# Optimization experiments

Measured on AMD Instinct MI355X. Metric: run time of the kernel, lower is better.

## Reference

```python
import jax, jax.numpy as jnp
import numpy as np
from itertools import combinations

B, F, E, V = 4096, 39, 40, 1000000
BN_EPS = 1e-3  # tf.layers.batch_normalization default epsilon


def setup_inputs() -> dict:
    key = jax.random.key(0)
    k_in, k_w, k_v, k_e = jax.random.split(key, 4)
    inputs = jax.random.randint(k_in, (B, F), 0, V, dtype=jnp.int64)
    # generate_pairs(range(F)): cols = first elements, rows = second elements
    pairs = np.array(list(combinations(range(F), 2)), dtype=np.int64)  # [741, 2]
    cols = jnp.asarray(pairs[:, 0])
    rows = jnp.asarray(pairs[:, 1])
    w = jax.random.normal(k_w, (V,), dtype=jnp.float32) * 0.01
    v = jax.random.normal(k_v, (V, E), dtype=jnp.float32) * (1.0 / np.sqrt(E))
    b = jnp.zeros((), dtype=jnp.float32)
    # edge weights init ~ uniform(weight_base - 1e-3, weight_base + 1e-3)
    edge_weights = jax.random.uniform(k_e, (pairs.shape[0],), dtype=jnp.float32,
                                      minval=0.599, maxval=0.601)
    return {"inputs": inputs, "rows": rows, "cols": cols,
            "w": w, "v": v, "b": b, "edge_weights": edge_weights}


def reference(inputs, rows, cols, w, v, b, edge_weights):
    # Embedding lookups
    xw = w[inputs]                      # [B, F]  first-order weights
    xv = v[inputs]                      # [B, F, E] second-order embeddings
    l = jnp.sum(xw, axis=1)             # [B] linear term

    # Pairwise FM interactions: gather field pairs, multiply, reduce over embed
    left = xv[:, rows]                  # [B, P, E]
    right = xv[:, cols]                 # [B, P, E]
    level_2 = jnp.sum(left * right, axis=-1)  # [B, P]

    # BatchNorm (training mode, scale=False, center=False): batch stats per pair
    mean = jnp.mean(level_2, axis=0)
    var = jnp.var(level_2, axis=0)      # biased variance, as in TF BN
    level_2 = (level_2 - mean) * jax.lax.rsqrt(var + BN_EPS)

    # Edge-weight (architecture) mask
    level_2 = level_2 * edge_weights[None, :]

    fm_out = jnp.sum(level_2, axis=-1)  # [B]
    logits = l + fm_out + b             # [B]
    return logits
```

## Files before the change

### kernel.cpp

```cpp
#include <hip/hip_runtime.h>

#define NF 39
#define NE 40
#define NB 4096
#define NSLOT 1536
#define NBLK 512
#define SPW 2
#define SPB 8
#define K2_BLOCKS 48
#define EPS 1.0e-3f

typedef __attribute__((ext_vector_type(8))) short short8;
typedef __attribute__((ext_vector_type(4))) float floatx4;

__device__ __forceinline__ unsigned int f2bf(float f) {
    unsigned int b = __float_as_uint(f);
    b += 0x7FFFu + ((b >> 16) & 1u);
    return b >> 16;
}

__device__ __forceinline__ short8 pack8(float4 a, float4 b) {
    union { unsigned int u[4]; short8 s; } o;
    o.u[0] = f2bf(a.x) | (f2bf(a.y) << 16);
    o.u[1] = f2bf(a.z) | (f2bf(a.w) << 16);
    o.u[2] = f2bf(b.x) | (f2bf(b.y) << 16);
    o.u[3] = f2bf(b.z) | (f2bf(b.w) << 16);
    return o.s;
}

__device__ __forceinline__ void load_frags(
    const int* __restrict__ ip, const float* __restrict__ v,
    int rbase, int ehalf, short8 F0[3], short8 F1[3])
{
    const float4 zero4 = {0.f, 0.f, 0.f, 0.f};
#pragma unroll
    for (int I = 0; I < 3; ++I) {
        const int r = rbase + 16 * I;
        const bool vr = (r < NF);
        const int id = vr ? ip[r] : 0;
        const float* vrow = v + (size_t)id * NE;
        const float4 a  = vr ? *reinterpret_cast<const float4*>(vrow + ehalf * 8)     : zero4;
        const float4 bq = vr ? *reinterpret_cast<const float4*>(vrow + ehalf * 8 + 4) : zero4;
        F0[I] = pack8(a, bq);
        const bool v1 = vr && (ehalf == 0);
        const float4 c_ = v1 ? *reinterpret_cast<const float4*>(vrow + 32) : zero4;
        const float4 d_ = v1 ? *reinterpret_cast<const float4*>(vrow + 36) : zero4;
        F1[I] = pack8(c_, d_);
    }
}

__device__ __forceinline__ void gram_mfma(const short8 F0[3], const short8 F1[3], floatx4 acc[6])
{
    acc[0] = __builtin_amdgcn_mfma_f32_16x16x32_bf16(F0[0], F0[0], acc[0], 0, 0, 0);
    acc[1] = __builtin_amdgcn_mfma_f32_16x16x32_bf16(F0[0], F0[1], acc[1], 0, 0, 0);
    acc[2] = __builtin_amdgcn_mfma_f32_16x16x32_bf16(F0[0], F0[2], acc[2], 0, 0, 0);
    acc[3] = __builtin_amdgcn_mfma_f32_16x16x32_bf16(F0[1], F0[1], acc[3], 0, 0, 0);
    acc[4] = __builtin_amdgcn_mfma_f32_16x16x32_bf16(F0[1], F0[2], acc[4], 0, 0, 0);
    acc[5] = __builtin_amdgcn_mfma_f32_16x16x32_bf16(F0[2], F0[2], acc[5], 0, 0, 0);
    acc[0] = __builtin_amdgcn_mfma_f32_16x16x32_bf16(F1[0], F1[0], acc[0], 0, 0, 0);
    acc[1] = __builtin_amdgcn_mfma_f32_16x16x32_bf16(F1[0], F1[1], acc[1], 0, 0, 0);
    acc[2] = __builtin_amdgcn_mfma_f32_16x16x32_bf16(F1[0], F1[2], acc[2], 0, 0, 0);
    acc[3] = __builtin_amdgcn_mfma_f32_16x16x32_bf16(F1[1], F1[1], acc[3], 0, 0, 0);
    acc[4] = __builtin_amdgcn_mfma_f32_16x16x32_bf16(F1[1], F1[2], acc[4], 0, 0, 0);
    acc[5] = __builtin_amdgcn_mfma_f32_16x16x32_bf16(F1[2], F1[2], acc[5], 0, 0, 0);
}

__global__ __launch_bounds__(256) void fm_k1(
    const int* __restrict__ inputs, const float* __restrict__ w,
    const float* __restrict__ v, short8* __restrict__ wf0,
    short8* __restrict__ wf1, float* __restrict__ lsum,
    float* __restrict__ partial)
{
    __shared__ float red[4 * 2 * NSLOT];
    const int t = threadIdx.x, wid = t >> 6, lane = t & 63;
    const int rbase = lane & 15, ehalf = lane >> 4;
    const int b0 = blockIdx.x * SPB;

    floatx4 sum[6] = {}, sq[6] = {};
#pragma unroll
    for (int s = 0; s < SPW; ++s) {
        const int smp = b0 + wid * SPW + s;
        const int* ip = inputs + (size_t)smp * NF;
        short8 F0[3], F1[3];
        load_frags(ip, v, rbase, ehalf, F0, F1);
#pragma unroll
        for (int I = 0; I < 3; ++I) {
            wf0[((size_t)smp * 3 + I) * 64 + lane] = F0[I];
            if (ehalf == 0) wf1[((size_t)smp * 3 + I) * 16 + rbase] = F1[I];
        }
        float wv = (lane < NF) ? w[ip[lane]] : 0.0f;
#pragma unroll
        for (int o = 32; o > 0; o >>= 1) wv += __shfl_down(wv, o, 64);
        if (lane == 0) lsum[smp] = wv;

        floatx4 acc[6] = {};
        gram_mfma(F0, F1, acc);
#pragma unroll
        for (int tl = 0; tl < 6; ++tl) {
            sum[tl] += acc[tl];
            sq[tl]  += acc[tl] * acc[tl];
        }
    }

    float* rw = &red[wid * 2 * NSLOT];
#pragma unroll
    for (int tl = 0; tl < 6; ++tl) {
        *reinterpret_cast<floatx4*>(rw + tl * 256 + lane * 4)         = sum[tl];
        *reinterpret_cast<floatx4*>(rw + NSLOT + tl * 256 + lane * 4) = sq[tl];
    }
    __syncthreads();
    float* po = partial + (size_t)blockIdx.x * (2 * NSLOT);
    for (int j = t; j < 2 * NSLOT; j += 256)
        po[j] = red[j] + red[2 * NSLOT + j] + red[4 * NSLOT + j] + red[6 * NSLOT + j];
}

__global__ __launch_bounds__(256) void fm_k2(
    const float* __restrict__ partial, const float* __restrict__ ew,
    float* __restrict__ meanArr, float* __restrict__ scaleArr)
{
    const int t = threadIdx.x;
    const int slotL = t & 31, rg = t >> 5;
    const int slot0 = blockIdx.x * 32;
    float s1 = 0.f, s2 = 0.f;
#pragma unroll 8
    for (int r = 0; r < 64; ++r) {
        const float* row = partial + (size_t)(rg * 64 + r) * (2 * NSLOT);
        s1 += row[slot0 + slotL];
        s2 += row[NSLOT + slot0 + slotL];
    }
    __shared__ float r1[8][32], r2[8][32];
    r1[rg][slotL] = s1;
    r2[rg][slotL] = s2;
    __syncthreads();
    if (t < 32) {
        float a = 0.f, b = 0.f;
#pragma unroll
        for (int g = 0; g < 8; ++g) { a += r1[g][t]; b += r2[g][t]; }
        const int slot = slot0 + t;
        const float m   = a * (1.0f / NB);
        const float var = b * (1.0f / NB) - m * m;
        const int tile = slot >> 8;
        const int l    = (slot & 255) >> 2;
        const int q    = slot & 3;
        const int TI[6] = {0, 0, 0, 1, 1, 2};
        const int TJ[6] = {0, 1, 2, 1, 2, 2};
        const int gi = 16 * TI[tile] + ((l >> 4) << 2) + q;
        const int gj = 16 * TJ[tile] + (l & 15);
        float scl = 0.0f;
        if (gi < gj && gj < NF) {
            const int p = 38 * gi - (gi * (gi - 1)) / 2 + (gj - gi - 1);
            scl = ew[p] * rsqrtf(var + EPS);
        }
        meanArr[slot]  = m;
        scaleArr[slot] = scl;
    }
}

__global__ __launch_bounds__(256) void fm_k3(
    const short8* __restrict__ wf0, const short8* __restrict__ wf1,
    const float* __restrict__ lsum, const float* __restrict__ meanArr,
    const float* __restrict__ scaleArr, const float* __restrict__ bias,
    float* __restrict__ out)
{
    const int t = threadIdx.x, wid = t >> 6, lane = t & 63;
    const int rbase = lane & 15, ehalf = lane >> 4;
    const int b0 = blockIdx.x * SPB;

    floatx4 mf[6], sf[6];
#pragma unroll
    for (int tl = 0; tl < 6; ++tl) {
        mf[tl] = *reinterpret_cast<const floatx4*>(meanArr  + tl * 256 + lane * 4);
        sf[tl] = *reinterpret_cast<const floatx4*>(scaleArr + tl * 256 + lane * 4);
    }
    const float bs = bias[0];
    const short8 z8 = {0, 0, 0, 0, 0, 0, 0, 0};

#pragma unroll
    for (int s = 0; s < SPW; ++s) {
        const int smp = b0 + wid * SPW + s;
        short8 F0[3], F1[3];
#pragma unroll
        for (int I = 0; I < 3; ++I) {
            F0[I] = wf0[((size_t)smp * 3 + I) * 64 + lane];
            F1[I] = (ehalf == 0) ? wf1[((size_t)smp * 3 + I) * 16 + rbase] : z8;
        }
        floatx4 acc[6] = {};
        gram_mfma(F0, F1, acc);
        float tot = (lane == 0) ? lsum[smp] : 0.0f;
#pragma unroll
        for (int tl = 0; tl < 6; ++tl)
#pragma unroll
            for (int q = 0; q < 4; ++q)
                tot += (acc[tl][q] - mf[tl][q]) * sf[tl][q];
#pragma unroll
        for (int o = 32; o > 0; o >>= 1) tot += __shfl_down(tot, o, 64);
        if (lane == 0) out[smp] = tot + bs;
    }
}

extern "C" void kernel_launch(void* const* d_in, const int* in_sizes, int n_in,
                              void* d_out, int out_size, void* d_ws, size_t ws_size,
                              hipStream_t stream)
{
    const int*   inputs = (const int*)  d_in[0];
    const float* w      = (const float*)d_in[3];
    const float* v      = (const float*)d_in[4];
    const float* bias   = (const float*)d_in[5];
    const float* ew     = (const float*)d_in[6];
    float*       out    = (float*)      d_out;

    short8* wf0 = (short8*)d_ws;
    short8* wf1 = wf0 + (size_t)NB * 3 * 64;
    float* partial = (float*)(wf1 + (size_t)NB * 3 * 16);
    float* meanA   = partial + (size_t)NBLK * 2 * NSLOT;
    float* scaleA  = meanA + NSLOT;
    float* lsum    = scaleA + NSLOT;

    fm_k1<<<NBLK,      256, 0, stream>>>(inputs, w, v, wf0, wf1, lsum, partial);
    fm_k2<<<K2_BLOCKS, 256, 0, stream>>>(partial, ew, meanA, scaleA);
    fm_k3<<<NBLK,      256, 0, stream>>>(wf0, wf1, lsum, meanA, scaleA, bias, out);
}
```

Before: 32.40 us.

## Split gather from Gram statistics into separate kernels for higher gather parallelism

The first kernel now only gathers the embedding rows, converts them to bf16 fragments and computes the linear sum, one sample per wave across 1024 blocks. It no longer holds the large LDS reduction buffer, so more waves can keep gathers in flight. A new kernel reloads the fragments from the workspace, recomputes the Gram MFMAs and writes per-block partial sums. This costs an extra launch and an extra read of the fragment buffer.

```diff
diff --git a/kernel.cpp b/kernel.cpp
--- a/kernel.cpp
+++ b/kernel.cpp
@@ -4,10 +4,10 @@
 #define NE 40
 #define NB 4096
 #define NSLOT 1536
-#define NBLK 512
-#define SPW 2
-#define SPB 8
-#define K2_BLOCKS 48
+#define K1_BLOCKS 1024
+#define K2A_BLOCKS 512
+#define K2B_BLOCKS 48
+#define K3_BLOCKS 512
 #define EPS 1.0e-3f
 
 typedef __attribute__((ext_vector_type(8))) short short8;
@@ -68,31 +68,46 @@
 __global__ __launch_bounds__(256) void fm_k1(
     const int* __restrict__ inputs, const float* __restrict__ w,
     const float* __restrict__ v, short8* __restrict__ wf0,
-    short8* __restrict__ wf1, float* __restrict__ lsum,
+    short8* __restrict__ wf1, float* __restrict__ lsum)
+{
+    const int t = threadIdx.x, wid = t >> 6, lane = t & 63;
+    const int rbase = lane & 15, ehalf = lane >> 4;
+    const int smp = blockIdx.x * 4 + wid;
+
+    const int* ip = inputs + (size_t)smp * NF;
+    short8 F0[3], F1[3];
+    load_frags(ip, v, rbase, ehalf, F0, F1);
+#pragma unroll
+    for (int I = 0; I < 3; ++I) {
+        wf0[((size_t)smp * 3 + I) * 64 + lane] = F0[I];
+        if (ehalf == 0) wf1[((size_t)smp * 3 + I) * 16 + rbase] = F1[I];
+    }
+    float wv = (lane < NF) ? w[ip[lane]] : 0.0f;
+#pragma unroll
+    for (int o = 32; o > 0; o >>= 1) wv += __shfl_down(wv, o, 64);
+    if (lane == 0) lsum[smp] = wv;
+}
+
+__global__ __launch_bounds__(256) void fm_k2a(
+    const short8* __restrict__ wf0, const short8* __restrict__ wf1,
     float* __restrict__ partial)
 {
     __shared__ float red[4 * 2 * NSLOT];
     const int t = threadIdx.x, wid = t >> 6, lane = t & 63;
     const int rbase = lane & 15, ehalf = lane >> 4;
-    const int b0 = blockIdx.x * SPB;
+    const int b0 = blockIdx.x * 8;
+    const short8 z8 = {0, 0, 0, 0, 0, 0, 0, 0};
 
     floatx4 sum[6] = {}, sq[6] = {};
 #pragma unroll
-    for (int s = 0; s < SPW; ++s) {
-        const int smp = b0 + wid * SPW + s;
-        const int* ip = inputs + (size_t)smp * NF;
+    for (int s = 0; s < 2; ++s) {
+        const int smp = b0 + wid * 2 + s;
         short8 F0[3], F1[3];
-        load_frags(ip, v, rbase, ehalf, F0, F1);
 #pragma unroll
         for (int I = 0; I < 3; ++I) {
-            wf0[((size_t)smp * 3 + I) * 64 + lane] = F0[I];
-            if (ehalf == 0) wf1[((size_t)smp * 3 + I) * 16 + rbase] = F1[I];
-        }
-        float wv = (lane < NF) ? w[ip[lane]] : 0.0f;
-#pragma unroll
-        for (int o = 32; o > 0; o >>= 1) wv += __shfl_down(wv, o, 64);
-        if (lane == 0) lsum[smp] = wv;
-
+            F0[I] = wf0[((size_t)smp * 3 + I) * 64 + lane];
+            F1[I] = (ehalf == 0) ? wf1[((size_t)smp * 3 + I) * 16 + rbase] : z8;
+        }
         floatx4 acc[6] = {};
         gram_mfma(F0, F1, acc);
 #pragma unroll
@@ -101,7 +116,6 @@
             sq[tl]  += acc[tl] * acc[tl];
         }
     }
-
     float* rw = &red[wid * 2 * NSLOT];
 #pragma unroll
     for (int tl = 0; tl < 6; ++tl) {
@@ -114,7 +128,7 @@
         po[j] = red[j] + red[2 * NSLOT + j] + red[4 * NSLOT + j] + red[6 * NSLOT + j];
 }
 
-__global__ __launch_bounds__(256) void fm_k2(
+__global__ __launch_bounds__(256) void fm_k2b(
     const float* __restrict__ partial, const float* __restrict__ ew,
     float* __restrict__ meanArr, float* __restrict__ scaleArr)
 {
@@ -164,7 +178,7 @@
 {
     const int t = threadIdx.x, wid = t >> 6, lane = t & 63;
     const int rbase = lane & 15, ehalf = lane >> 4;
-    const int b0 = blockIdx.x * SPB;
+    const int b0 = blockIdx.x * 8;
 
     floatx4 mf[6], sf[6];
 #pragma unroll
@@ -176,8 +190,8 @@
     const short8 z8 = {0, 0, 0, 0, 0, 0, 0, 0};
 
 #pragma unroll
-    for (int s = 0; s < SPW; ++s) {
-        const int smp = b0 + wid * SPW + s;
+    for (int s = 0; s < 2; ++s) {
+        const int smp = b0 + wid * 2 + s;
         short8 F0[3], F1[3];
 #pragma unroll
         for (int I = 0; I < 3; ++I) {
@@ -212,11 +226,12 @@
     short8* wf0 = (short8*)d_ws;
     short8* wf1 = wf0 + (size_t)NB * 3 * 64;
     float* partial = (float*)(wf1 + (size_t)NB * 3 * 16);
-    float* meanA   = partial + (size_t)NBLK * 2 * NSLOT;
+    float* meanA   = partial + (size_t)K2A_BLOCKS * 2 * NSLOT;
     float* scaleA  = meanA + NSLOT;
     float* lsum    = scaleA + NSLOT;
 
-    fm_k1<<<NBLK,      256, 0, stream>>>(inputs, w, v, wf0, wf1, lsum, partial);
-    fm_k2<<<K2_BLOCKS, 256, 0, stream>>>(partial, ew, meanA, scaleA);
-    fm_k3<<<NBLK,      256, 0, stream>>>(wf0, wf1, lsum, meanA, scaleA, bias, out);
-}
+    fm_k1 <<<K1_BLOCKS,  256, 0, stream>>>(inputs, w, v, wf0, wf1, lsum);
+    fm_k2a<<<K2A_BLOCKS, 256, 0, stream>>>(wf0, wf1, partial);
+    fm_k2b<<<K2B_BLOCKS, 256, 0, stream>>>(partial, ew, meanA, scaleA);
+    fm_k3 <<<K3_BLOCKS,  256, 0, stream>>>(wf0, wf1, lsum, meanA, scaleA, bias, out);
+}
```

New measurement: 34.79 us. 7.4% more time.

## Materialize bf16 Gram matrix instead of recomputing it from stored fragments

Applied to the files above, without the earlier changes.

The first kernel now writes each sample's pairwise Gram tile as bf16, instead of storing embedding fragments and per-block sum/sumsq partials. The stats kernel reduces directly over all 4096 rows of this matrix, and the final kernel reads it back instead of redoing the MFMA gram. This removes the recomputation and the partial-sum staging, but the stats kernel now streams the full matrix with few blocks. Rounding to bf16 before computing mean and variance also reduces precision.

```diff
diff --git a/kernel.cpp b/kernel.cpp
--- a/kernel.cpp
+++ b/kernel.cpp
@@ -17,6 +17,10 @@
     unsigned int b = __float_as_uint(f);
     b += 0x7FFFu + ((b >> 16) & 1u);
     return b >> 16;
+}
+
+__device__ __forceinline__ float bf2f(unsigned int u) {
+    return __uint_as_float(u << 16);
 }
 
 __device__ __forceinline__ short8 pack8(float4 a, float4 b) {
@@ -67,27 +71,20 @@
 
 __global__ __launch_bounds__(256) void fm_k1(
     const int* __restrict__ inputs, const float* __restrict__ w,
-    const float* __restrict__ v, short8* __restrict__ wf0,
-    short8* __restrict__ wf1, float* __restrict__ lsum,
-    float* __restrict__ partial)
-{
-    __shared__ float red[4 * 2 * NSLOT];
+    const float* __restrict__ v, unsigned short* __restrict__ Gb,
+    float* __restrict__ lsum)
+{
     const int t = threadIdx.x, wid = t >> 6, lane = t & 63;
     const int rbase = lane & 15, ehalf = lane >> 4;
     const int b0 = blockIdx.x * SPB;
 
-    floatx4 sum[6] = {}, sq[6] = {};
 #pragma unroll
     for (int s = 0; s < SPW; ++s) {
         const int smp = b0 + wid * SPW + s;
         const int* ip = inputs + (size_t)smp * NF;
         short8 F0[3], F1[3];
         load_frags(ip, v, rbase, ehalf, F0, F1);
-#pragma unroll
-        for (int I = 0; I < 3; ++I) {
-            wf0[((size_t)smp * 3 + I) * 64 + lane] = F0[I];
-            if (ehalf == 0) wf1[((size_t)smp * 3 + I) * 16 + rbase] = F1[I];
-        }
+
         float wv = (lane < NF) ? w[ip[lane]] : 0.0f;
 #pragma unroll
         for (int o = 32; o > 0; o >>= 1) wv += __shfl_down(wv, o, 64);
@@ -95,27 +92,20 @@
 
         floatx4 acc[6] = {};
         gram_mfma(F0, F1, acc);
+
+        unsigned short* gr = Gb + (size_t)smp * NSLOT;
 #pragma unroll
         for (int tl = 0; tl < 6; ++tl) {
-            sum[tl] += acc[tl];
-            sq[tl]  += acc[tl] * acc[tl];
+            uint2 pk;
+            pk.x = f2bf(acc[tl][0]) | (f2bf(acc[tl][1]) << 16);
+            pk.y = f2bf(acc[tl][2]) | (f2bf(acc[tl][3]) << 16);
+            *reinterpret_cast<uint2*>(gr + tl * 256 + lane * 4) = pk;
         }
     }
-
-    float* rw = &red[wid * 2 * NSLOT];
-#pragma unroll
-    for (int tl = 0; tl < 6; ++tl) {
-        *reinterpret_cast<floatx4*>(rw + tl * 256 + lane * 4)         = sum[tl];
-        *reinterpret_cast<floatx4*>(rw + NSLOT + tl * 256 + lane * 4) = sq[tl];
-    }
-    __syncthreads();
-    float* po = partial + (size_t)blockIdx.x * (2 * NSLOT);
-    for (int j = t; j < 2 * NSLOT; j += 256)
-        po[j] = red[j] + red[2 * NSLOT + j] + red[4 * NSLOT + j] + red[6 * NSLOT + j];
-}
-
-__global__ __launch_bounds__(256) void fm_k2(
-    const float* __restrict__ partial, const float* __restrict__ ew,
+}
+
+__global__ __launch_bounds__(512) void fm_k2(
+    const unsigned short* __restrict__ Gb, const float* __restrict__ ew,
     float* __restrict__ meanArr, float* __restrict__ scaleArr)
 {
     const int t = threadIdx.x;
@@ -123,19 +113,20 @@
     const int slot0 = blockIdx.x * 32;
     float s1 = 0.f, s2 = 0.f;
 #pragma unroll 8
-    for (int r = 0; r < 64; ++r) {
-        const float* row = partial + (size_t)(rg * 64 + r) * (2 * NSLOT);
-        s1 += row[slot0 + slotL];
-        s2 += row[NSLOT + slot0 + slotL];
-    }
-    __shared__ float r1[8][32], r2[8][32];
+    for (int r = 0; r < 256; ++r) {
+        const int row = rg * 256 + r;
+        const float x = bf2f(Gb[(size_t)row * NSLOT + slot0 + slotL]);
+        s1 += x;
+        s2 = fmaf(x, x, s2);
+    }
+    __shared__ float r1[16][32], r2[16][32];
     r1[rg][slotL] = s1;
     r2[rg][slotL] = s2;
     __syncthreads();
     if (t < 32) {
         float a = 0.f, b = 0.f;
 #pragma unroll
-        for (int g = 0; g < 8; ++g) { a += r1[g][t]; b += r2[g][t]; }
+        for (int g = 0; g < 16; ++g) { a += r1[g][t]; b += r2[g][t]; }
         const int slot = slot0 + t;
         const float m   = a * (1.0f / NB);
         const float var = b * (1.0f / NB) - m * m;
@@ -157,13 +148,11 @@
 }
 
 __global__ __launch_bounds__(256) void fm_k3(
-    const short8* __restrict__ wf0, const short8* __restrict__ wf1,
-    const float* __restrict__ lsum, const float* __restrict__ meanArr,
-    const float* __restrict__ scaleArr, const float* __restrict__ bias,
-    float* __restrict__ out)
+    const unsigned short* __restrict__ Gb, const float* __restrict__ lsum,
+    const float* __restrict__ meanArr, const float* __restrict__ scaleArr,
+    const float* __restrict__ bias, float* __restrict__ out)
 {
     const int t = threadIdx.x, wid = t >> 6, lane = t & 63;
-    const int rbase = lane & 15, ehalf = lane >> 4;
     const int b0 = blockIdx.x * SPB;
 
     floatx4 mf[6], sf[6];
@@ -173,25 +162,24 @@
         sf[tl] = *reinterpret_cast<const floatx4*>(scaleArr + tl * 256 + lane * 4);
     }
     const float bs = bias[0];
-    const short8 z8 = {0, 0, 0, 0, 0, 0, 0, 0};
 
 #pragma unroll
     for (int s = 0; s < SPW; ++s) {
         const int smp = b0 + wid * SPW + s;
-        short8 F0[3], F1[3];
-#pragma unroll
-        for (int I = 0; I < 3; ++I) {
-            F0[I] = wf0[((size_t)smp * 3 + I) * 64 + lane];
-            F1[I] = (ehalf == 0) ? wf1[((size_t)smp * 3 + I) * 16 + rbase] : z8;
+        const unsigned short* gr = Gb + (size_t)smp * NSLOT;
+        float tot = (lane == 0) ? lsum[smp] : 0.0f;
+#pragma unroll
+        for (int tl = 0; tl < 6; ++tl) {
+            const uint2 pk = *reinterpret_cast<const uint2*>(gr + tl * 256 + lane * 4);
+            const float g0 = bf2f(pk.x & 0xFFFFu);
+            const float g1 = bf2f(pk.x >> 16);
+            const float g2 = bf2f(pk.y & 0xFFFFu);
+            const float g3 = bf2f(pk.y >> 16);
+            tot += (g0 - mf[tl][0]) * sf[tl][0];
+            tot += (g1 - mf[tl][1]) * sf[tl][1];
+            tot += (g2 - mf[tl][2]) * sf[tl][2];
+            tot += (g3 - mf[tl][3]) * sf[tl][3];
         }
-        floatx4 acc[6] = {};
-        gram_mfma(F0, F1, acc);
-        float tot = (lane == 0) ? lsum[smp] : 0.0f;
-#pragma unroll
-        for (int tl = 0; tl < 6; ++tl)
-#pragma unroll
-            for (int q = 0; q < 4; ++q)
-                tot += (acc[tl][q] - mf[tl][q]) * sf[tl][q];
 #pragma unroll
         for (int o = 32; o > 0; o >>= 1) tot += __shfl_down(tot, o, 64);
         if (lane == 0) out[smp] = tot + bs;
@@ -209,14 +197,12 @@
     const float* ew     = (const float*)d_in[6];
     float*       out    = (float*)      d_out;
 
-    short8* wf0 = (short8*)d_ws;
-    short8* wf1 = wf0 + (size_t)NB * 3 * 64;
-    float* partial = (float*)(wf1 + (size_t)NB * 3 * 16);
-    float* meanA   = partial + (size_t)NBLK * 2 * NSLOT;
-    float* scaleA  = meanA + NSLOT;
-    float* lsum    = scaleA + NSLOT;
-
-    fm_k1<<<NBLK,      256, 0, stream>>>(inputs, w, v, wf0, wf1, lsum, partial);
-    fm_k2<<<K2_BLOCKS, 256, 0, stream>>>(partial, ew, meanA, scaleA);
-    fm_k3<<<NBLK,      256, 0, stream>>>(wf0, wf1, lsum, meanA, scaleA, bias, out);
-}
+    unsigned short* Gb = (unsigned short*)d_ws;
+    float* lsum   = (float*)(Gb + (size_t)NB * NSLOT);
+    float* meanA  = lsum + NB;
+    float* scaleA = meanA + NSLOT;
+
+    fm_k1<<<NBLK,      256, 0, stream>>>(inputs, w, v, Gb, lsum);
+    fm_k2<<<K2_BLOCKS, 512, 0, stream>>>(Gb, ew, meanA, scaleA);
+    fm_k3<<<NBLK,      256, 0, stream>>>(Gb, lsum, meanA, scaleA, bias, out);
+}
```

After: 36.41 us. +12.4%, slower.
